# Performance work log

Measured on AMD Instinct MI355X. Metric: run time of the kernel, lower is better.

Reference implementation:

```python
import jax, jax.numpy as jnp
import numpy as np

NUM_HEADS = 16
NEG_FILL = -10000.0  # matches torch masked_fill value in source


def setup_inputs() -> dict:
    key = jax.random.key(0)
    ks = jax.random.split(key, 8)
    B, S, H = 4, 2048, 1024
    sc = 1.0 / np.sqrt(H)
    x = jax.random.normal(ks[0], (B, S, H), dtype=jnp.float32)
    L = jax.random.randint(ks[1], (B,), 1, S + 1, dtype=jnp.int64 if jax.config.jax_enable_x64 else jnp.int32)
    Wq = jax.random.normal(ks[2], (H, H), dtype=jnp.float32) * sc
    Wk = jax.random.normal(ks[3], (H, H), dtype=jnp.float32) * sc
    Wv = jax.random.normal(ks[4], (H, H), dtype=jnp.float32) * sc
    bv = jax.random.normal(ks[5], (H,), dtype=jnp.float32) * 0.01
    Wo = jax.random.normal(ks[6], (H, H), dtype=jnp.float32) * sc
    bo = jax.random.normal(ks[7], (H,), dtype=jnp.float32) * 0.01
    return {"x": x, "L": L, "Wq": Wq, "Wk": Wk, "Wv": Wv, "bv": bv, "Wo": Wo, "bo": bo}


def reference(x, L, Wq, Wk, Wv, bv, Wo, bo):
    # AttentionAggregator.forward with L given; dropout in eval mode (identity).
    B, S, H = x.shape
    nh = NUM_HEADS
    dk = H // nh
    # torch nn.Linear: y = x @ W.T + b
    q = (x @ Wq.T).reshape(B, S, nh, dk).transpose(0, 2, 1, 3)  # (B,h,S,dk)
    k = (x @ Wk.T).reshape(B, S, nh, dk).transpose(0, 2, 1, 3)
    v = (x @ Wv.T + bv).reshape(B, S, nh, dk).transpose(0, 2, 1, 3)
    scores = jnp.einsum("bhqd,bhkd->bhqk", q, k) / jnp.sqrt(jnp.float32(dk))
    valid = jnp.arange(S)[None, :] < L[:, None]  # (B,S) True where real token
    scores = jnp.where(valid[:, None, None, :], scores, NEG_FILL)
    attn = jax.nn.softmax(scores, axis=-1)
    ctx = jnp.einsum("bhqk,bhkd->bhqd", attn, v)
    ctx = ctx.transpose(0, 2, 1, 3).reshape(B, S, H)
    attn_out = ctx @ Wo.T + bo  # (B,S,H)
    # masked mean pool over valid positions
    m = valid.astype(x.dtype)  # (B,S)
    pooled = jnp.einsum("bsh,bs->bh", attn_out, m) / m.sum(axis=1, keepdims=True)
    return pooled
```

## Files before the change

kernel.cpp:

```cpp
#include <hip/hip_runtime.h>
#include <hip/hip_bf16.h>
#include <math.h>

constexpr int Bc = 4, Sc = 2048, Hc = 1024, NHc = 16, DKc = 64;

constexpr size_t XHOFF = 0;
constexpr size_t QOFF  = 4194304;
constexpr size_t KOFF  = 8388608;
constexpr size_t WQOFF = 12582912;
constexpr size_t WKOFF = 13107200;
constexpr size_t LIOFF = 13631488;
constexpr size_t WOFF  = 13762560;
constexpr size_t YOFF  = 13893632;
constexpr size_t CSOFF = 13959168;
constexpr size_t YPOFF = 13963264;
constexpr size_t RPOFF = 13963264;
constexpr size_t CPOFF = 13963264;

typedef __attribute__((ext_vector_type(8))) short bf16x8;
typedef __attribute__((ext_vector_type(4))) float f32x4;

__device__ inline short f2bf(float v) {
    __hip_bfloat16 h = __float2bfloat16(v);
    return *reinterpret_cast<short*>(&h);
}

__device__ inline float ex2(float x) {
#if defined(__has_builtin) && __has_builtin(__builtin_amdgcn_exp2f)
    return __builtin_amdgcn_exp2f(x);
#else
    float r; asm("v_exp_f32 %0, %1" : "=v"(r) : "v"(x)); return r;
#endif
}

__device__ inline void gld_lds16(const void* g, void* l) {
    __builtin_amdgcn_global_load_lds(
        (const __attribute__((address_space(1))) unsigned int*)g,
        (__attribute__((address_space(3))) unsigned int*)l, 16, 0, 0);
}

__global__ __launch_bounds__(256) void cvt_all_kernel(
    const float* __restrict__ x, const float* __restrict__ Wq,
    const float* __restrict__ Wk, float* __restrict__ ws)
{
    const size_t i = ((size_t)blockIdx.x * 256 + threadIdx.x) * 8;
    const float* src; short* dst; float scale; size_t off;
    constexpr float QSC = 0.125f * 1.44269504088896340736f;
    if (i < 8388608)       { src = x;  dst = (short*)(ws + XHOFF); off = i;            scale = 1.0f; }
    else if (i < 9437184)  { src = Wq; dst = (short*)(ws + WQOFF); off = i - 8388608;  scale = QSC;  }
    else                   { src = Wk; dst = (short*)(ws + WKOFF); off = i - 9437184;  scale = 1.0f; }
    float4 a = *(const float4*)(src + off);
    float4 b = *(const float4*)(src + off + 4);
    bf16x8 o;
    o[0] = f2bf(a.x * scale); o[1] = f2bf(a.y * scale);
    o[2] = f2bf(a.z * scale); o[3] = f2bf(a.w * scale);
    o[4] = f2bf(b.x * scale); o[5] = f2bf(b.y * scale);
    o[6] = f2bf(b.z * scale); o[7] = f2bf(b.w * scale);
    *(bf16x8*)(dst + off) = o;
}

__global__ __launch_bounds__(256) void proj_mfma_kernel(
    const int* __restrict__ L, float* __restrict__ ws)
{
    const int z  = blockIdx.z;
    const int m0 = blockIdx.y * 128;
    const int n0 = blockIdx.x * 128;
    const int b  = m0 >> 11;
    const int s0 = m0 & 2047;
    const int Lb = L[b];
    if (s0 >= Lb) return;

    const short* __restrict__ A = (const short*)(ws + XHOFF);
    const short* __restrict__ W = (const short*)(ws + (z == 0 ? WQOFF : WKOFF));
    short* __restrict__ Out = (short*)(ws + (z == 0 ? QOFF : KOFF));

    __shared__ __align__(16) short As[128 * 32];
    __shared__ __align__(16) short Bs[128 * 32];

    const int tid  = threadIdx.x;
    const int lane = tid & 63;
    const int wave = tid >> 6;
    const int l16  = lane & 15, quad = lane >> 4;
    const int wm = (wave & 1) * 64, wn = (wave >> 1) * 64;

    const int c0 = tid, c1 = tid + 256;
    const int r0 = c0 >> 2, g0 = (c0 & 3) * 8;
    const int r1 = c1 >> 2, g1 = (c1 & 3) * 8;
    short* lA0 = As + wave * 512;
    short* lA1 = As + 2048 + wave * 512;
    short* lB0 = Bs + wave * 512;
    short* lB1 = Bs + 2048 + wave * 512;

    const f32x4 z4 = {0.f, 0.f, 0.f, 0.f};
    f32x4 acc[4][4];
    #pragma unroll
    for (int i = 0; i < 4; ++i)
        #pragma unroll
        for (int j = 0; j < 4; ++j) acc[i][j] = z4;

    for (int k0 = 0; k0 < Hc; k0 += 32) {
        __syncthreads();
        gld_lds16(A + (size_t)(m0 + r0) * Hc + k0 + g0, lA0);
        gld_lds16(A + (size_t)(m0 + r1) * Hc + k0 + g1, lA1);
        gld_lds16(W + (size_t)(n0 + r0) * Hc + k0 + g0, lB0);
        gld_lds16(W + (size_t)(n0 + r1) * Hc + k0 + g1, lB1);
        __syncthreads();

        bf16x8 af[4], bfr[4];
        #pragma unroll
        for (int mt = 0; mt < 4; ++mt)
            af[mt] = *(const bf16x8*)(As + (wm + mt * 16 + l16) * 32 + quad * 8);
        #pragma unroll
        for (int nt = 0; nt < 4; ++nt)
            bfr[nt] = *(const bf16x8*)(Bs + (wn + nt * 16 + l16) * 32 + quad * 8);
        #pragma unroll
        for (int mt = 0; mt < 4; ++mt)
            #pragma unroll
            for (int nt = 0; nt < 4; ++nt)
                acc[mt][nt] = __builtin_amdgcn_mfma_f32_16x16x32_bf16(
                    af[mt], bfr[nt], acc[mt][nt], 0, 0, 0);
    }

    #pragma unroll
    for (int mt = 0; mt < 4; ++mt) {
        #pragma unroll
        for (int nt = 0; nt < 4; ++nt) {
            const int n = n0 + wn + nt * 16 + l16;
            const int h = n >> 6, d = n & 63;
            #pragma unroll
            for (int r = 0; r < 4; ++r) {
                const int s = s0 + wm + mt * 16 + quad * 4 + r;
                Out[(((size_t)b * NHc + h) * Sc + s) * DKc + d] =
                    f2bf(acc[mt][nt][r]);
            }
        }
    }
}

__global__ __launch_bounds__(256) void rowsum_part_kernel(
    const int* __restrict__ L, float* __restrict__ ws)
{
    const int bh = blockIdx.x;
    const int b  = bh >> 4;
    const int Lb = L[b];
    const int kc0 = blockIdx.z * 128;
    if (blockIdx.y * 128 >= Lb || kc0 >= Lb) return;

    const int tid  = threadIdx.x;
    const int wave = tid >> 6;
    const int lane = tid & 63;
    const int q0 = blockIdx.y * 128 + wave * 32;
    const int l16 = lane & 15, quad = lane >> 4;

    const short* __restrict__ qarr = (const short*)(ws + QOFF) + (size_t)bh * Sc * DKc;
    const short* __restrict__ karr = (const short*)(ws + KOFF) + (size_t)bh * Sc * DKc;

    __shared__ __align__(16) short Ks[128 * 64];

    const short* qrow0 = qarr + (size_t)(q0 + l16) * DKc;
    const short* qrow1 = qarr + (size_t)(q0 + 16 + l16) * DKc;
    const bf16x8 b0lo = *(const bf16x8*)(qrow0 + quad * 8);
    const bf16x8 b0hi = *(const bf16x8*)(qrow0 + 32 + quad * 8);
    const bf16x8 b1lo = *(const bf16x8*)(qrow1 + quad * 8);
    const bf16x8 b1hi = *(const bf16x8*)(qrow1 + 32 + quad * 8);

    #pragma unroll
    for (int i = 0; i < 4; ++i) {
        const int s = i * 256 + tid;
        const int row = s >> 3, cc = s & 7, c = cc ^ (row & 7);
        gld_lds16(karr + (size_t)(kc0 + row) * DKc + c * 8,
                  Ks + (i * 256 + wave * 64) * 8);
    }
    __syncthreads();

    float lacc0 = 0.f, lacc1 = 0.f;
    if (kc0 + 128 <= Lb) {
        #pragma unroll
        for (int t = 0; t < 8; ++t) {
            const int r = t * 16 + l16;
            const bf16x8 alo = *(const bf16x8*)(Ks + (r * 8 + (quad ^ (r & 7))) * 8);
            const bf16x8 ahi = *(const bf16x8*)(Ks + (r * 8 + ((4 + quad) ^ (r & 7))) * 8);
            f32x4 c0 = {0.f, 0.f, 0.f, 0.f}, c1 = {0.f, 0.f, 0.f, 0.f};
            c0 = __builtin_amdgcn_mfma_f32_16x16x32_bf16(alo, b0lo, c0, 0, 0, 0);
            c0 = __builtin_amdgcn_mfma_f32_16x16x32_bf16(ahi, b0hi, c0, 0, 0, 0);
            c1 = __builtin_amdgcn_mfma_f32_16x16x32_bf16(alo, b1lo, c1, 0, 0, 0);
            c1 = __builtin_amdgcn_mfma_f32_16x16x32_bf16(ahi, b1hi, c1, 0, 0, 0);
            const float e0 = ex2(c0[0]), e1 = ex2(c0[1]), e2 = ex2(c0[2]), e3 = ex2(c0[3]);
            const float f0 = ex2(c1[0]), f1 = ex2(c1[1]), f2 = ex2(c1[2]), f3 = ex2(c1[3]);
            lacc0 += (e0 + e1) + (e2 + e3);
            lacc1 += (f0 + f1) + (f2 + f3);
        }
    } else {
        #pragma unroll
        for (int t = 0; t < 8; ++t) {
            const int r = t * 16 + l16;
            const bf16x8 alo = *(const bf16x8*)(Ks + (r * 8 + (quad ^ (r & 7))) * 8);
            const bf16x8 ahi = *(const bf16x8*)(Ks + (r * 8 + ((4 + quad) ^ (r & 7))) * 8);
            f32x4 c0 = {0.f, 0.f, 0.f, 0.f}, c1 = {0.f, 0.f, 0.f, 0.f};
            c0 = __builtin_amdgcn_mfma_f32_16x16x32_bf16(alo, b0lo, c0, 0, 0, 0);
            c0 = __builtin_amdgcn_mfma_f32_16x16x32_bf16(ahi, b0hi, c0, 0, 0, 0);
            c1 = __builtin_amdgcn_mfma_f32_16x16x32_bf16(alo, b1lo, c1, 0, 0, 0);
            c1 = __builtin_amdgcn_mfma_f32_16x16x32_bf16(ahi, b1hi, c1, 0, 0, 0);
            #pragma unroll
            for (int rr = 0; rr < 4; ++rr) {
                const bool kv = (kc0 + t * 16 + quad * 4 + rr) < Lb;
                lacc0 += kv ? ex2(c0[rr]) : 0.f;
                lacc1 += kv ? ex2(c1[rr]) : 0.f;
            }
        }
    }
    lacc0 += __shfl_xor(lacc0, 16, 64); lacc0 += __shfl_xor(lacc0, 32, 64);
    lacc1 += __shfl_xor(lacc1, 16, 64); lacc1 += __shfl_xor(lacc1, 32, 64);
    float* __restrict__ rp = ws + RPOFF + ((size_t)blockIdx.z * 64 + bh) * Sc;
    if (quad == 0) rp[q0 + l16]      = lacc0;
    if (quad == 1) rp[q0 + 16 + l16] = lacc1;
}

__global__ __launch_bounds__(256) void rowsum_reduce_kernel(
    const int* __restrict__ L, float* __restrict__ ws)
{
    const int bh = blockIdx.y;
    const int q  = blockIdx.x * 256 + threadIdx.x;
    const int nc = (L[bh >> 4] + 127) >> 7;
    float acc = 0.f;
    for (int c = 0; c < nc; ++c)
        acc += ws[RPOFF + ((size_t)c * 64 + bh) * Sc + q];
    ws[LIOFF + (size_t)bh * Sc + q] = 1.0f / acc;
}

__global__ __launch_bounds__(256) void colsum_part_kernel(
    const int* __restrict__ L, float* __restrict__ ws)
{
    const int bh = blockIdx.x;
    const int b  = bh >> 4;
    const int Lb = L[b];
    const int qc0 = blockIdx.z * 128;
    if (blockIdx.y * 128 >= Lb || qc0 >= Lb) return;

    const int tid  = threadIdx.x;
    const int wave = tid >> 6;
    const int lane = tid & 63;
    const int k0 = blockIdx.y * 128 + wave * 32;
    const int l16 = lane & 15, quad = lane >> 4;

    const short* __restrict__ qarr = (const short*)(ws + QOFF) + (size_t)bh * Sc * DKc;
    const short* __restrict__ karr = (const short*)(ws + KOFF) + (size_t)bh * Sc * DKc;
    const float* __restrict__ liarr = ws + LIOFF + (size_t)bh * Sc;

    __shared__ __align__(16) short Qs[128 * 64];
    __shared__ __align__(16) float Lis[128];

    const short* krow0 = karr + (size_t)(k0 + l16) * DKc;
    const short* krow1 = karr + (size_t)(k0 + 16 + l16) * DKc;
    const bf16x8 a0lo = *(const bf16x8*)(krow0 + quad * 8);
    const bf16x8 a0hi = *(const bf16x8*)(krow0 + 32 + quad * 8);
    const bf16x8 a1lo = *(const bf16x8*)(krow1 + quad * 8);
    const bf16x8 a1hi = *(const bf16x8*)(krow1 + 32 + quad * 8);

    #pragma unroll
    for (int i = 0; i < 4; ++i) {
        const int s = i * 256 + tid;
        const int row = s >> 3, cc = s & 7, c = cc ^ (row & 7);
        gld_lds16(qarr + (size_t)(qc0 + row) * DKc + c * 8,
                  Qs + (i * 256 + wave * 64) * 8);
    }
    if (tid < 32)
        gld_lds16(liarr + qc0 + tid * 4, Lis);
    __syncthreads();

    float w0[4] = {0.f, 0.f, 0.f, 0.f};
    float w1[4] = {0.f, 0.f, 0.f, 0.f};

    if (qc0 + 128 <= Lb) {
        #pragma unroll
        for (int t = 0; t < 8; ++t) {
            const int r = t * 16 + l16;
            const bf16x8 blo = *(const bf16x8*)(Qs + (r * 8 + (quad ^ (r & 7))) * 8);
            const bf16x8 bhi = *(const bf16x8*)(Qs + (r * 8 + ((4 + quad) ^ (r & 7))) * 8);
            const float lv = Lis[r];
            f32x4 c0 = {0.f, 0.f, 0.f, 0.f}, c1 = {0.f, 0.f, 0.f, 0.f};
            c0 = __builtin_amdgcn_mfma_f32_16x16x32_bf16(a0lo, blo, c0, 0, 0, 0);
            c0 = __builtin_amdgcn_mfma_f32_16x16x32_bf16(a0hi, bhi, c0, 0, 0, 0);
            c1 = __builtin_amdgcn_mfma_f32_16x16x32_bf16(a1lo, blo, c1, 0, 0, 0);
            c1 = __builtin_amdgcn_mfma_f32_16x16x32_bf16(a1hi, bhi, c1, 0, 0, 0);
            #pragma unroll
            for (int rr = 0; rr < 4; ++rr) {
                w0[rr] += ex2(c0[rr]) * lv;
                w1[rr] += ex2(c1[rr]) * lv;
            }
        }
    } else {
        #pragma unroll
        for (int t = 0; t < 8; ++t) {
            const int r = t * 16 + l16;
            const bf16x8 blo = *(const bf16x8*)(Qs + (r * 8 + (quad ^ (r & 7))) * 8);
            const bf16x8 bhi = *(const bf16x8*)(Qs + (r * 8 + ((4 + quad) ^ (r & 7))) * 8);
            const float lv = (qc0 + r < Lb) ? Lis[r] : 0.f;
            f32x4 c0 = {0.f, 0.f, 0.f, 0.f}, c1 = {0.f, 0.f, 0.f, 0.f};
            c0 = __builtin_amdgcn_mfma_f32_16x16x32_bf16(a0lo, blo, c0, 0, 0, 0);
            c0 = __builtin_amdgcn_mfma_f32_16x16x32_bf16(a0hi, bhi, c0, 0, 0, 0);
            c1 = __builtin_amdgcn_mfma_f32_16x16x32_bf16(a1lo, blo, c1, 0, 0, 0);
            c1 = __builtin_amdgcn_mfma_f32_16x16x32_bf16(a1hi, bhi, c1, 0, 0, 0);
            #pragma unroll
            for (int rr = 0; rr < 4; ++rr) {
                w0[rr] += ex2(c0[rr]) * lv;
                w1[rr] += ex2(c1[rr]) * lv;
            }
        }
    }
    #pragma unroll
    for (int off = 1; off <= 8; off <<= 1) {
        #pragma unroll
        for (int rr = 0; rr < 4; ++rr) {
            w0[rr] += __shfl_xor(w0[rr], off, 64);
            w1[rr] += __shfl_xor(w1[rr], off, 64);
        }
    }
    if (l16 == 0) {
        float* __restrict__ cp = ws + CPOFF + ((size_t)blockIdx.z * 64 + bh) * Sc;
        #pragma unroll
        for (int rr = 0; rr < 4; ++rr) {
            cp[k0 + quad * 4 + rr]      = w0[rr];
            cp[k0 + 16 + quad * 4 + rr] = w1[rr];
        }
    }
}

__global__ __launch_bounds__(256) void colsum_reduce_kernel(
    const int* __restrict__ L, float* __restrict__ ws)
{
    const int bh = blockIdx.y;
    const int k  = blockIdx.x * 256 + threadIdx.x;
    const int nc = (L[bh >> 4] + 127) >> 7;
    float acc = 0.f;
    for (int c = 0; c < nc; ++c)
        acc += ws[CPOFF + ((size_t)c * 64 + bh) * Sc + k];
    ws[WOFF + (size_t)bh * Sc + k] = acc;
}

__global__ __launch_bounds__(256) void yw_part_kernel(
    const float* __restrict__ x, const int* __restrict__ L,
    float* __restrict__ ws)
{
    const int b  = blockIdx.y;
    const int j0 = blockIdx.x * 64;
    const int s0 = blockIdx.z * 128;
    const int Lb = L[b];
    if (s0 >= Lb) return;
    const int js = threadIdx.x & 63;
    const int sl = threadIdx.x >> 6;
    const float* __restrict__ warr = ws + WOFF + (size_t)b * NHc * Sc;
    const float* __restrict__ xb = x + (size_t)b * Sc * Hc;

    __shared__ float wt[128][20];
    __shared__ float red[4][16][64];

    #pragma unroll
    for (int i = 0; i < 8; ++i) {
        const int s = (threadIdx.x & 15) + 16 * i;
        const int h = threadIdx.x >> 4;
        float v = 0.f;
        if (s0 + s < Lb) v = warr[(size_t)h * Sc + s0 + s];
        wt[s][h] = v;
    }
    __syncthreads();

    float acc[16];
    #pragma unroll
    for (int h = 0; h < 16; ++h) acc[h] = 0.f;

    #pragma unroll 4
    for (int s = sl; s < 128; s += 4) {
        const float xv = xb[(size_t)(s0 + s) * Hc + j0 + js];
        const f32x4 wa = *(const f32x4*)&wt[s][0];
        const f32x4 wb = *(const f32x4*)&wt[s][4];
        const f32x4 wc = *(const f32x4*)&wt[s][8];
        const f32x4 wd = *(const f32x4*)&wt[s][12];
        #pragma unroll
        for (int h = 0; h < 4; ++h) acc[h]      += wa[h] * xv;
        #pragma unroll
        for (int h = 0; h < 4; ++h) acc[4 + h]  += wb[h] * xv;
        #pragma unroll
        for (int h = 0; h < 4; ++h) acc[8 + h]  += wc[h] * xv;
        #pragma unroll
        for (int h = 0; h < 4; ++h) acc[12 + h] += wd[h] * xv;
    }
    #pragma unroll
    for (int h = 0; h < 16; ++h) red[sl][h][js] = acc[h];
    __syncthreads();
    if (sl == 0) {
        float* __restrict__ yp = ws + YPOFF +
            ((size_t)blockIdx.z * Bc * NHc + (size_t)b * NHc) * Hc;
        #pragma unroll
        for (int h = 0; h < 16; ++h)
            yp[(size_t)h * Hc + j0 + js] =
                red[0][h][js] + red[1][h][js] + red[2][h][js] + red[3][h][js];
    }
}

__global__ __launch_bounds__(256) void yw_reduce_kernel(
    const int* __restrict__ L, float* __restrict__ ws)
{
    const int b = blockIdx.y;
    const int i = blockIdx.x * 256 + threadIdx.x;
    const int nc = (L[b] + 127) >> 7;
    const float* __restrict__ p = ws + YPOFF + (size_t)b * NHc * Hc + i;
    float acc = 0.f;
    for (int c = 0; c < nc; ++c)
        acc += p[(size_t)c * Bc * NHc * Hc];
    ws[YOFF + (size_t)b * NHc * Hc + i] = acc;
}

__global__ __launch_bounds__(256) void csum_kernel(
    const float* __restrict__ Wv, const float* __restrict__ bv,
    const int* __restrict__ L, float* __restrict__ ws)
{
    const int b = blockIdx.y;
    const int h = blockIdx.x;
    const int n0 = h * 64;
    const int lane = threadIdx.x & 63;
    const int wave = threadIdx.x >> 6;
    const float Lb = (float)L[b];

    __shared__ float ys[1024];
    const float* __restrict__ y = ws + YOFF + ((size_t)b * NHc + h) * Hc;
    for (int i = threadIdx.x; i < 1024; i += 256) ys[i] = y[i];
    __syncthreads();

    f32x4 yv[4];
    #pragma unroll
    for (int p = 0; p < 4; ++p) yv[p] = *(const f32x4*)&ys[p * 256 + lane * 4];

    #pragma unroll
    for (int r = 0; r < 16; ++r) {
        const int n = n0 + wave * 16 + r;
        const float* wrow = Wv + (size_t)n * Hc;
        float a = 0.f;
        #pragma unroll
        for (int p = 0; p < 4; ++p) {
            const f32x4 wv = *(const f32x4*)(wrow + p * 256 + lane * 4);
            a += wv[0]*yv[p][0] + wv[1]*yv[p][1] + wv[2]*yv[p][2] + wv[3]*yv[p][3];
        }
        #pragma unroll
        for (int off = 32; off > 0; off >>= 1) a += __shfl_xor(a, off, 64);
        if (lane == 0)
            ws[CSOFF + (size_t)b * Hc + n] = a + bv[n] * Lb;
    }
}

__global__ __launch_bounds__(256) void out_kernel(
    const float* __restrict__ Wo, const float* __restrict__ bo,
    const int* __restrict__ L, const float* __restrict__ ws,
    float* __restrict__ out)
{
    const int b = blockIdx.y;
    const int o0 = blockIdx.x * 64;
    const int lane = threadIdx.x & 63;
    const int wave = threadIdx.x >> 6;
    const float linv = 1.0f / (float)L[b];

    __shared__ float cs[1024];
    const float* __restrict__ c = ws + CSOFF + (size_t)b * Hc;
    for (int i = threadIdx.x; i < 1024; i += 256) cs[i] = c[i];
    __syncthreads();

    f32x4 cv[4];
    #pragma unroll
    for (int p = 0; p < 4; ++p) cv[p] = *(const f32x4*)&cs[p * 256 + lane * 4];

    #pragma unroll
    for (int r = 0; r < 16; ++r) {
        const int o = o0 + wave * 16 + r;
        const float* wrow = Wo + (size_t)o * Hc;
        float a = 0.f;
        #pragma unroll
        for (int p = 0; p < 4; ++p) {
            const f32x4 wv = *(const f32x4*)(wrow + p * 256 + lane * 4);
            a += wv[0]*cv[p][0] + wv[1]*cv[p][1] + wv[2]*cv[p][2] + wv[3]*cv[p][3];
        }
        #pragma unroll
        for (int off = 32; off > 0; off >>= 1) a += __shfl_xor(a, off, 64);
        if (lane == 0)
            out[(size_t)b * Hc + o] = a * linv + bo[o];
    }
}

extern "C" void kernel_launch(void* const* d_in, const int* in_sizes, int n_in,
                              void* d_out, int out_size, void* d_ws, size_t ws_size,
                              hipStream_t stream)
{
    (void)in_sizes; (void)n_in; (void)out_size; (void)ws_size;
    const float* x  = (const float*)d_in[0];
    const int*   L  = (const int*)d_in[1];
    const float* Wq = (const float*)d_in[2];
    const float* Wk = (const float*)d_in[3];
    const float* Wv = (const float*)d_in[4];
    const float* bv = (const float*)d_in[5];
    const float* Wo = (const float*)d_in[6];
    const float* bo = (const float*)d_in[7];
    float* out = (float*)d_out;
    float* ws  = (float*)d_ws;

    cvt_all_kernel<<<5120, 256, 0, stream>>>(x, Wq, Wk, ws);

    dim3 gp(Hc / 128, (Bc * Sc) / 128, 2);
    proj_mfma_kernel<<<gp, 256, 0, stream>>>(L, ws);

    dim3 gr(Bc * NHc, Sc / 128, 16);
    rowsum_part_kernel<<<gr, 256, 0, stream>>>(L, ws);
    dim3 grr(Sc / 256, Bc * NHc);
    rowsum_reduce_kernel<<<grr, 256, 0, stream>>>(L, ws);

    dim3 gcp(Bc * NHc, Sc / 128, 16);
    colsum_part_kernel<<<gcp, 256, 0, stream>>>(L, ws);
    colsum_reduce_kernel<<<grr, 256, 0, stream>>>(L, ws);

    dim3 gy(Hc / 64, Bc, Sc / 128);
    yw_part_kernel<<<gy, 256, 0, stream>>>(x, L, ws);

    dim3 gyr((NHc * Hc) / 256, Bc);
    yw_reduce_kernel<<<gyr, 256, 0, stream>>>(L, ws);

    dim3 gc(NHc, Bc);
    csum_kernel<<<gc, 256, 0, stream>>>(Wv, bv, L, ws);

    dim3 go(Hc / 64, Bc);
    out_kernel<<<go, 256, 0, stream>>>(Wo, bo, L, ws, out);
}
```

Before: 240.9 us.

## Keep key/query tiles in registers and loop over the other axis in rowsum/colsum

```diff
diff --git a/kernel.cpp b/kernel.cpp
--- a/kernel.cpp
+++ b/kernel.cpp
@@ -137,83 +137,79 @@
     }
 }
 
-__global__ __launch_bounds__(256) void rowsum_part_kernel(
+__global__ __launch_bounds__(256, 4) void rowsum_part_kernel(
     const int* __restrict__ L, float* __restrict__ ws)
 {
     const int bh = blockIdx.x;
+    const int zc = blockIdx.y;
     const int b  = bh >> 4;
     const int Lb = L[b];
-    const int kc0 = blockIdx.z * 128;
-    if (blockIdx.y * 128 >= Lb || kc0 >= Lb) return;
-
-    const int tid  = threadIdx.x;
-    const int wave = tid >> 6;
-    const int lane = tid & 63;
-    const int q0 = blockIdx.y * 128 + wave * 32;
+    const int kt = zc * 128;
+    if (kt >= Lb) return;
+
+    const int lane = threadIdx.x & 63;
+    const int wave = threadIdx.x >> 6;
     const int l16 = lane & 15, quad = lane >> 4;
 
     const short* __restrict__ qarr = (const short*)(ws + QOFF) + (size_t)bh * Sc * DKc;
     const short* __restrict__ karr = (const short*)(ws + KOFF) + (size_t)bh * Sc * DKc;
 
-    __shared__ __align__(16) short Ks[128 * 64];
-
-    const short* qrow0 = qarr + (size_t)(q0 + l16) * DKc;
-    const short* qrow1 = qarr + (size_t)(q0 + 16 + l16) * DKc;
-    const bf16x8 b0lo = *(const bf16x8*)(qrow0 + quad * 8);
-    const bf16x8 b0hi = *(const bf16x8*)(qrow0 + 32 + quad * 8);
-    const bf16x8 b1lo = *(const bf16x8*)(qrow1 + quad * 8);
-    const bf16x8 b1hi = *(const bf16x8*)(qrow1 + 32 + quad * 8);
-
-    #pragma unroll
-    for (int i = 0; i < 4; ++i) {
-        const int s = i * 256 + tid;
-        const int row = s >> 3, cc = s & 7, c = cc ^ (row & 7);
-        gld_lds16(karr + (size_t)(kc0 + row) * DKc + c * 8,
-                  Ks + (i * 256 + wave * 64) * 8);
-    }
-    __syncthreads();
-
-    float lacc0 = 0.f, lacc1 = 0.f;
-    if (kc0 + 128 <= Lb) {
-        #pragma unroll
-        for (int t = 0; t < 8; ++t) {
-            const int r = t * 16 + l16;
-            const bf16x8 alo = *(const bf16x8*)(Ks + (r * 8 + (quad ^ (r & 7))) * 8);
-            const bf16x8 ahi = *(const bf16x8*)(Ks + (r * 8 + ((4 + quad) ^ (r & 7))) * 8);
-            f32x4 c0 = {0.f, 0.f, 0.f, 0.f}, c1 = {0.f, 0.f, 0.f, 0.f};
-            c0 = __builtin_amdgcn_mfma_f32_16x16x32_bf16(alo, b0lo, c0, 0, 0, 0);
-            c0 = __builtin_amdgcn_mfma_f32_16x16x32_bf16(ahi, b0hi, c0, 0, 0, 0);
-            c1 = __builtin_amdgcn_mfma_f32_16x16x32_bf16(alo, b1lo, c1, 0, 0, 0);
-            c1 = __builtin_amdgcn_mfma_f32_16x16x32_bf16(ahi, b1hi, c1, 0, 0, 0);
-            const float e0 = ex2(c0[0]), e1 = ex2(c0[1]), e2 = ex2(c0[2]), e3 = ex2(c0[3]);
-            const float f0 = ex2(c1[0]), f1 = ex2(c1[1]), f2 = ex2(c1[2]), f3 = ex2(c1[3]);
-            lacc0 += (e0 + e1) + (e2 + e3);
-            lacc1 += (f0 + f1) + (f2 + f3);
-        }
-    } else {
-        #pragma unroll
-        for (int t = 0; t < 8; ++t) {
-            const int r = t * 16 + l16;
-            const bf16x8 alo = *(const bf16x8*)(Ks + (r * 8 + (quad ^ (r & 7))) * 8);
-            const bf16x8 ahi = *(const bf16x8*)(Ks + (r * 8 + ((4 + quad) ^ (r & 7))) * 8);
-            f32x4 c0 = {0.f, 0.f, 0.f, 0.f}, c1 = {0.f, 0.f, 0.f, 0.f};
-            c0 = __builtin_amdgcn_mfma_f32_16x16x32_bf16(alo, b0lo, c0, 0, 0, 0);
-            c0 = __builtin_amdgcn_mfma_f32_16x16x32_bf16(ahi, b0hi, c0, 0, 0, 0);
-            c1 = __builtin_amdgcn_mfma_f32_16x16x32_bf16(alo, b1lo, c1, 0, 0, 0);
-            c1 = __builtin_amdgcn_mfma_f32_16x16x32_bf16(ahi, b1hi, c1, 0, 0, 0);
-            #pragma unroll
-            for (int rr = 0; rr < 4; ++rr) {
-                const bool kv = (kc0 + t * 16 + quad * 4 + rr) < Lb;
-                lacc0 += kv ? ex2(c0[rr]) : 0.f;
-                lacc1 += kv ? ex2(c1[rr]) : 0.f;
+    bf16x8 ka[8][2];
+    #pragma unroll
+    for (int tt = 0; tt < 8; ++tt) {
+        const short* kr = karr + (size_t)(kt + tt * 16 + l16) * DKc;
+        ka[tt][0] = *(const bf16x8*)(kr + quad * 8);
+        ka[tt][1] = *(const bf16x8*)(kr + 32 + quad * 8);
+    }
+
+    const bool full = (kt + 128 <= Lb);
+    const int nq = (Lb + 127) >> 7;
+    float* __restrict__ rp = ws + RPOFF + ((size_t)zc * 64 + bh) * Sc;
+
+    for (int y = 0; y < nq; ++y) {
+        const int q0 = y * 128 + wave * 32;
+        const short* qrow0 = qarr + (size_t)(q0 + l16) * DKc;
+        const short* qrow1 = qarr + (size_t)(q0 + 16 + l16) * DKc;
+        const bf16x8 b0lo = *(const bf16x8*)(qrow0 + quad * 8);
+        const bf16x8 b0hi = *(const bf16x8*)(qrow0 + 32 + quad * 8);
+        const bf16x8 b1lo = *(const bf16x8*)(qrow1 + quad * 8);
+        const bf16x8 b1hi = *(const bf16x8*)(qrow1 + 32 + quad * 8);
+
+        float lacc0 = 0.f, lacc1 = 0.f;
+        if (full) {
+            #pragma unroll
+            for (int tt = 0; tt < 8; ++tt) {
+                f32x4 c0 = {0.f, 0.f, 0.f, 0.f}, c1 = {0.f, 0.f, 0.f, 0.f};
+                c0 = __builtin_amdgcn_mfma_f32_16x16x32_bf16(ka[tt][0], b0lo, c0, 0, 0, 0);
+                c0 = __builtin_amdgcn_mfma_f32_16x16x32_bf16(ka[tt][1], b0hi, c0, 0, 0, 0);
+                c1 = __builtin_amdgcn_mfma_f32_16x16x32_bf16(ka[tt][0], b1lo, c1, 0, 0, 0);
+                c1 = __builtin_amdgcn_mfma_f32_16x16x32_bf16(ka[tt][1], b1hi, c1, 0, 0, 0);
+                const float e0 = ex2(c0[0]), e1 = ex2(c0[1]), e2 = ex2(c0[2]), e3 = ex2(c0[3]);
+                const float f0 = ex2(c1[0]), f1 = ex2(c1[1]), f2 = ex2(c1[2]), f3 = ex2(c1[3]);
+                lacc0 += (e0 + e1) + (e2 + e3);
+                lacc1 += (f0 + f1) + (f2 + f3);
             }
-        }
-    }
-    lacc0 += __shfl_xor(lacc0, 16, 64); lacc0 += __shfl_xor(lacc0, 32, 64);
-    lacc1 += __shfl_xor(lacc1, 16, 64); lacc1 += __shfl_xor(lacc1, 32, 64);
-    float* __restrict__ rp = ws + RPOFF + ((size_t)blockIdx.z * 64 + bh) * Sc;
-    if (quad == 0) rp[q0 + l16]      = lacc0;
-    if (quad == 1) rp[q0 + 16 + l16] = lacc1;
+        } else {
+            #pragma unroll
+            for (int tt = 0; tt < 8; ++tt) {
+                f32x4 c0 = {0.f, 0.f, 0.f, 0.f}, c1 = {0.f, 0.f, 0.f, 0.f};
+                c0 = __builtin_amdgcn_mfma_f32_16x16x32_bf16(ka[tt][0], b0lo, c0, 0, 0, 0);
+                c0 = __builtin_amdgcn_mfma_f32_16x16x32_bf16(ka[tt][1], b0hi, c0, 0, 0, 0);
+                c1 = __builtin_amdgcn_mfma_f32_16x16x32_bf16(ka[tt][0], b1lo, c1, 0, 0, 0);
+                c1 = __builtin_amdgcn_mfma_f32_16x16x32_bf16(ka[tt][1], b1hi, c1, 0, 0, 0);
+                #pragma unroll
+                for (int rr = 0; rr < 4; ++rr) {
+                    const bool kv = (kt + tt * 16 + quad * 4 + rr) < Lb;
+                    lacc0 += kv ? ex2(c0[rr]) : 0.f;
+                    lacc1 += kv ? ex2(c1[rr]) : 0.f;
+                }
+            }
+        }
+        lacc0 += __shfl_xor(lacc0, 16, 64); lacc0 += __shfl_xor(lacc0, 32, 64);
+        lacc1 += __shfl_xor(lacc1, 16, 64); lacc1 += __shfl_xor(lacc1, 32, 64);
+        if (quad == 0) rp[q0 + l16]      = lacc0;
+        if (quad == 1) rp[q0 + 16 + l16] = lacc1;
+    }
 }
 
 __global__ __launch_bounds__(256) void rowsum_reduce_kernel(
@@ -228,100 +224,77 @@
     ws[LIOFF + (size_t)bh * Sc + q] = 1.0f / acc;
 }
 
-__global__ __launch_bounds__(256) void colsum_part_kernel(
+__global__ __launch_bounds__(256, 4) void colsum_part_kernel(
     const int* __restrict__ L, float* __restrict__ ws)
 {
     const int bh = blockIdx.x;
+    const int zq = blockIdx.y;
     const int b  = bh >> 4;
     const int Lb = L[b];
-    const int qc0 = blockIdx.z * 128;
-    if (blockIdx.y * 128 >= Lb || qc0 >= Lb) return;
-
-    const int tid  = threadIdx.x;
-    const int wave = tid >> 6;
-    const int lane = tid & 63;
-    const int k0 = blockIdx.y * 128 + wave * 32;
+    const int qt = zq * 128;
+    if (qt >= Lb) return;
+
+    const int lane = threadIdx.x & 63;
+    const int wave = threadIdx.x >> 6;
     const int l16 = lane & 15, quad = lane >> 4;
 
     const short* __restrict__ qarr = (const short*)(ws + QOFF) + (size_t)bh * Sc * DKc;
     const short* __restrict__ karr = (const short*)(ws + KOFF) + (size_t)bh * Sc * DKc;
-    const float* __restrict__ liarr = ws + LIOFF + (size_t)bh * Sc;
-
-    __shared__ __align__(16) short Qs[128 * 64];
-    __shared__ __align__(16) float Lis[128];
-
-    const short* krow0 = karr + (size_t)(k0 + l16) * DKc;
-    const short* krow1 = karr + (size_t)(k0 + 16 + l16) * DKc;
-    const bf16x8 a0lo = *(const bf16x8*)(krow0 + quad * 8);
-    const bf16x8 a0hi = *(const bf16x8*)(krow0 + 32 + quad * 8);
-    const bf16x8 a1lo = *(const bf16x8*)(krow1 + quad * 8);
-    const bf16x8 a1hi = *(const bf16x8*)(krow1 + 32 + quad * 8);
-
-    #pragma unroll
-    for (int i = 0; i < 4; ++i) {
-        const int s = i * 256 + tid;
-        const int row = s >> 3, cc = s & 7, c = cc ^ (row & 7);
-        gld_lds16(qarr + (size_t)(qc0 + row) * DKc + c * 8,
-                  Qs + (i * 256 + wave * 64) * 8);
-    }
-    if (tid < 32)
-        gld_lds16(liarr + qc0 + tid * 4, Lis);
-    __syncthreads();
-
-    float w0[4] = {0.f, 0.f, 0.f, 0.f};
-    float w1[4] = {0.f, 0.f, 0.f, 0.f};
-
-    if (qc0 + 128 <= Lb) {
-        #pragma unroll
-        for (int t = 0; t < 8; ++t) {
-            const int r = t * 16 + l16;
-            const bf16x8 blo = *(const bf16x8*)(Qs + (r * 8 + (quad ^ (r & 7))) * 8);
-            const bf16x8 bhi = *(const bf16x8*)(Qs + (r * 8 + ((4 + quad) ^ (r & 7))) * 8);
-            const float lv = Lis[r];
+    const float* __restrict__ li = ws + LIOFF + (size_t)bh * Sc;
+
+    bf16x8 qb[8][2];
+    float lv[8];
+    #pragma unroll
+    for (int tt = 0; tt < 8; ++tt) {
+        const int qrow = qt + tt * 16 + l16;
+        const short* qr = qarr + (size_t)qrow * DKc;
+        qb[tt][0] = *(const bf16x8*)(qr + quad * 8);
+        qb[tt][1] = *(const bf16x8*)(qr + 32 + quad * 8);
+        lv[tt] = (qrow < Lb) ? li[qrow] : 0.f;
+    }
+
+    const int nk = (Lb + 127) >> 7;
+    float* __restrict__ cp = ws + CPOFF + ((size_t)zq * 64 + bh) * Sc;
+
+    for (int yk = 0; yk < nk; ++yk) {
+        const int k0 = yk * 128 + wave * 32;
+        const short* krow0 = karr + (size_t)(k0 + l16) * DKc;
+        const short* krow1 = karr + (size_t)(k0 + 16 + l16) * DKc;
+        const bf16x8 a0lo = *(const bf16x8*)(krow0 + quad * 8);
+        const bf16x8 a0hi = *(const bf16x8*)(krow0 + 32 + quad * 8);
+        const bf16x8 a1lo = *(const bf16x8*)(krow1 + quad * 8);
+        const bf16x8 a1hi = *(const bf16x8*)(krow1 + 32 + quad * 8);
+
+        float w0[4] = {0.f, 0.f, 0.f, 0.f};
+        float w1[4] = {0.f, 0.f, 0.f, 0.f};
+        #pragma unroll
+        for (int tt = 0; tt < 8; ++tt) {
             f32x4 c0 = {0.f, 0.f, 0.f, 0.f}, c1 = {0.f, 0.f, 0.f, 0.f};
-            c0 = __builtin_amdgcn_mfma_f32_16x16x32_bf16(a0lo, blo, c0, 0, 0, 0);
-            c0 = __builtin_amdgcn_mfma_f32_16x16x32_bf16(a0hi, bhi, c0, 0, 0, 0);
-            c1 = __builtin_amdgcn_mfma_f32_16x16x32_bf16(a1lo, blo, c1, 0, 0, 0);
-            c1 = __builtin_amdgcn_mfma_f32_16x16x32_bf16(a1hi, bhi, c1, 0, 0, 0);
+            c0 = __builtin_amdgcn_mfma_f32_16x16x32_bf16(a0lo, qb[tt][0], c0, 0, 0, 0);
+            c0 = __builtin_amdgcn_mfma_f32_16x16x32_bf16(a0hi, qb[tt][1], c0, 0, 0, 0);
+            c1 = __builtin_amdgcn_mfma_f32_16x16x32_bf16(a1lo, qb[tt][0], c1, 0, 0, 0);
+            c1 = __builtin_amdgcn_mfma_f32_16x16x32_bf16(a1hi, qb[tt][1], c1, 0, 0, 0);
+            const float lvt = lv[tt];
             #pragma unroll
             for (int rr = 0; rr < 4; ++rr) {
-                w0[rr] += ex2(c0[rr]) * lv;
-                w1[rr] += ex2(c1[rr]) * lv;
+                w0[rr] += ex2(c0[rr]) * lvt;
+                w1[rr] += ex2(c1[rr]) * lvt;
             }
         }
-    } else {
-        #pragma unroll
-        for (int t = 0; t < 8; ++t) {
-            const int r = t * 16 + l16;
-            const bf16x8 blo = *(const bf16x8*)(Qs + (r * 8 + (quad ^ (r & 7))) * 8);
-            const bf16x8 bhi = *(const bf16x8*)(Qs + (r * 8 + ((4 + quad) ^ (r & 7))) * 8);
-            const float lv = (qc0 + r < Lb) ? Lis[r] : 0.f;
-            f32x4 c0 = {0.f, 0.f, 0.f, 0.f}, c1 = {0.f, 0.f, 0.f, 0.f};
-            c0 = __builtin_amdgcn_mfma_f32_16x16x32_bf16(a0lo, blo, c0, 0, 0, 0);
-            c0 = __builtin_amdgcn_mfma_f32_16x16x32_bf16(a0hi, bhi, c0, 0, 0, 0);
-            c1 = __builtin_amdgcn_mfma_f32_16x16x32_bf16(a1lo, blo, c1, 0, 0, 0);
-            c1 = __builtin_amdgcn_mfma_f32_16x16x32_bf16(a1hi, bhi, c1, 0, 0, 0);
+        #pragma unroll
+        for (int off = 1; off <= 8; off <<= 1) {
             #pragma unroll
             for (int rr = 0; rr < 4; ++rr) {
-                w0[rr] += ex2(c0[rr]) * lv;
-                w1[rr] += ex2(c1[rr]) * lv;
+                w0[rr] += __shfl_xor(w0[rr], off, 64);
+                w1[rr] += __shfl_xor(w1[rr], off, 64);
             }
         }
-    }
-    #pragma unroll
-    for (int off = 1; off <= 8; off <<= 1) {
-        #pragma unroll
-        for (int rr = 0; rr < 4; ++rr) {
-            w0[rr] += __shfl_xor(w0[rr], off, 64);
-            w1[rr] += __shfl_xor(w1[rr], off, 64);
-        }
-    }
-    if (l16 == 0) {
-        float* __restrict__ cp = ws + CPOFF + ((size_t)blockIdx.z * 64 + bh) * Sc;
-        #pragma unroll
-        for (int rr = 0; rr < 4; ++rr) {
-            cp[k0 + quad * 4 + rr]      = w0[rr];
-            cp[k0 + 16 + quad * 4 + rr] = w1[rr];
+        if (l16 == 0) {
+            #pragma unroll
+            for (int rr = 0; rr < 4; ++rr) {
+                cp[k0 + quad * 4 + rr]      = w0[rr];
+                cp[k0 + 16 + quad * 4 + rr] = w1[rr];
+            }
         }
     }
 }
@@ -506,13 +479,12 @@
     dim3 gp(Hc / 128, (Bc * Sc) / 128, 2);
     proj_mfma_kernel<<<gp, 256, 0, stream>>>(L, ws);
 
-    dim3 gr(Bc * NHc, Sc / 128, 16);
+    dim3 gr(Bc * NHc, Sc / 128);
     rowsum_part_kernel<<<gr, 256, 0, stream>>>(L, ws);
     dim3 grr(Sc / 256, Bc * NHc);
     rowsum_reduce_kernel<<<grr, 256, 0, stream>>>(L, ws);
 
-    dim3 gcp(Bc * NHc, Sc / 128, 16);
-    colsum_part_kernel<<<gcp, 256, 0, stream>>>(L, ws);
+    colsum_part_kernel<<<gr, 256, 0, stream>>>(L, ws);
     colsum_reduce_kernel<<<grr, 256, 0, stream>>>(L, ws);
 
     dim3 gy(Hc / 64, Bc, Sc / 128);
```

After: 391.0 us. 62.3% more time.
